# Kernel tuning notes

Measured on AMD Instinct MI355X. Metric: run time of the kernel, lower is better.

## Reference

```python
import jax, jax.numpy as jnp
import numpy as np

B, H, L, D = 2, 16, 2048, 64


def setup_inputs() -> dict:
    key = jax.random.key(0)
    kq, kk, kv = jax.random.split(key, 3)
    queries = jax.random.normal(kq, (B, H, L, D), dtype=jnp.float32)
    keys = jax.random.normal(kk, (B, H, L, D), dtype=jnp.float32)
    values = jax.random.normal(kv, (B, H, L, D), dtype=jnp.float32)
    # causal mask: True = masked (as consumed by masked_fill in the original)
    attn_mask = jnp.triu(jnp.ones((L, L), dtype=bool), k=1)
    return {"queries": queries, "keys": keys, "values": values, "attn_mask": attn_mask}


def reference(queries, keys, values, attn_mask):
    D_ = queries.shape[-1]
    scale = 1.0 / jnp.sqrt(jnp.asarray(D_, dtype=queries.dtype))
    # [B,H,Lq,Lk] score matrix (faithfully materialized as in the original)
    scores = jnp.einsum("bhqd,bhkd->bhqk", queries, keys) * scale
    scores = jnp.where(attn_mask, jnp.asarray(-1e9, dtype=scores.dtype), scores)
    attention = jax.nn.softmax(scores, axis=-1)
    # dropout rate = 0.0 (inference); identity
    out = jnp.einsum("bhqk,bhkd->bhqd", attention, values)
    return out
```

## Files before the change

### kernel.cpp

```cpp
#include <hip/hip_runtime.h>


constexpr int Lq = 2048;
constexpr int Dh = 64;
constexpr int TILEB = 16384;
constexpr int VOFF  = 8192;
constexpr size_t CNT_OFF = (size_t)32 * 32 * TILEB;
constexpr int JOBS_PER_CLASS = 256;

typedef __attribute__((ext_vector_type(16))) float f32x16;
typedef __attribute__((ext_vector_type(4))) float f32x4;
typedef __attribute__((ext_vector_type(8))) unsigned short u16x8;
typedef __attribute__((ext_vector_type(4))) unsigned int u32x4;
typedef __attribute__((ext_vector_type(8))) __bf16 bf16x8;

__device__ __forceinline__ unsigned short f2bf(float f) {
  __bf16 h = (__bf16)f;
  return __builtin_bit_cast(unsigned short, h);
}
__device__ __forceinline__ unsigned cvtpk(float lo, float hi) {
  unsigned r;
  asm("v_cvt_pk_bf16_f32 %0, %1, %2" : "=v"(r) : "v"(lo), "v"(hi));
  return r;
}
__device__ __forceinline__ f32x16 mfma32(u16x8 a, u16x8 b, f32x16 c) {
  return __builtin_amdgcn_mfma_f32_32x32x16_bf16(
      __builtin_bit_cast(bf16x8, a), __builtin_bit_cast(bf16x8, b), c, 0, 0, 0);
}
__device__ __forceinline__ void plswap(unsigned a, unsigned b,
                                       unsigned& wlo, unsigned& whi) {
#if __has_builtin(__builtin_amdgcn_permlane32_swap)
  auto r = __builtin_amdgcn_permlane32_swap((int)a, (int)b, false, false);
  wlo = (unsigned)r[0];
  whi = (unsigned)r[1];
#else
  const int hh = (threadIdx.x >> 5) & 1;
  unsigned pa = (unsigned)__shfl_xor((int)a, 32);
  unsigned pb = (unsigned)__shfl_xor((int)b, 32);
  wlo = hh ? pb : a;
  whi = hh ? b : pa;
#endif
}

__global__ __launch_bounds__(256, 2)
void repack(const float* __restrict__ K, const float* __restrict__ V,
            unsigned char* __restrict__ W, int* cnt) {
  __shared__ unsigned short Vl[64][72];

  if (cnt && blockIdx.x == 0 && threadIdx.x < 8) cnt[threadIdx.x * 64] = 0;

  const int tid = threadIdx.x;
  const int bt  = blockIdx.x;
  const int bh  = bt >> 5;
  const int tl  = bt & 31;
  const size_t src = (size_t)bh * Lq * Dh + (size_t)tl * 64 * Dh;
  unsigned char* img = W + (size_t)bt * TILEB;

  const int r  = tid >> 2;
  const int c2 = (tid & 3) * 2;

  {
    const float* kp = K + src + (size_t)r * Dh + c2 * 8;
    f32x4 a = *(const f32x4*)kp;
    f32x4 b = *(const f32x4*)(kp + 4);
    f32x4 c = *(const f32x4*)(kp + 8);
    f32x4 d = *(const f32x4*)(kp + 12);
    u16x8 lo, hi;
    #pragma unroll
    for (int jj = 0; jj < 4; ++jj) {
      lo[jj] = f2bf(a[jj]); lo[4 + jj] = f2bf(b[jj]);
      hi[jj] = f2bf(c[jj]); hi[4 + jj] = f2bf(d[jj]);
    }
    *(u16x8*)(img + (c2 * 64 + r) * 16)       = lo;
    *(u16x8*)(img + ((c2 + 1) * 64 + r) * 16) = hi;
  }
  {
    const float* vp = V + src + (size_t)r * Dh + c2 * 8;
    f32x4 a = *(const f32x4*)vp;
    f32x4 b = *(const f32x4*)(vp + 4);
    f32x4 c = *(const f32x4*)(vp + 8);
    f32x4 d = *(const f32x4*)(vp + 12);
    u16x8 lo, hi;
    #pragma unroll
    for (int jj = 0; jj < 4; ++jj) {
      lo[jj] = f2bf(a[jj]); lo[4 + jj] = f2bf(b[jj]);
      hi[jj] = f2bf(c[jj]); hi[4 + jj] = f2bf(d[jj]);
    }
    *(u16x8*)&Vl[r][c2 * 8]     = lo;
    *(u16x8*)&Vl[r][c2 * 8 + 8] = hi;
  }
  __syncthreads();
  {
    u16x8 lo, hi;
    #pragma unroll
    for (int e = 0; e < 8; ++e) {
      lo[e] = Vl[c2 * 8 + e][r];
      hi[e] = Vl[c2 * 8 + 8 + e][r];
    }
    *(u16x8*)(img + VOFF + (c2 * 64 + r) * 16)       = lo;
    *(u16x8*)(img + VOFF + ((c2 + 1) * 64 + r) * 16) = hi;
  }
}

__global__ __launch_bounds__(256, 4)
void fattn_fwd(const float* __restrict__ Q, const unsigned char* __restrict__ W,
               float* __restrict__ O, int* cnt) {
  __shared__ float Mrg[64][33];
  __shared__ int jobLDS;

  const int tid  = threadIdx.x;
  const int lane = tid & 63;
  const int w    = tid >> 6;
  const int l31  = lane & 31;
  const int h    = lane >> 5;

  const int cls  = blockIdx.x & 7;
  int* qcnt = cnt ? (cnt + cls * 64) : nullptr;

  const float QS = 0.125f * 1.4426950408889634f;
  const int laneK = ((w & 1) * 32 + l31) * 16 + h * 1024;
  const int laneV = VOFF + ((w & 1) * 4 + h) * 1024 + l31 * 16;

  for (;;) {
    int j;
    if (qcnt) {
      if (tid == 0) jobLDS = atomicAdd(qcnt, 1);
      __syncthreads();
      j = jobLDS;
    } else {
      j = blockIdx.x >> 3;
    }
    if (j >= JOBS_PER_CLASS) break;

    const int qg   = 63 - (j >> 2);
    const int bh   = cls * 4 + (j & 3);
    const int qmin = qg * 32;
    const size_t base = (size_t)bh * Lq * Dh;

    u16x8 qc[4];
    {
      const float* qp = Q + base + (size_t)(qmin + l31) * Dh + h * 8;
      #pragma unroll
      for (int dc = 0; dc < 4; ++dc) {
        f32x4 lo = *(const f32x4*)(qp + dc * 16);
        f32x4 hi = *(const f32x4*)(qp + dc * 16 + 4);
        u16x8 f;
        #pragma unroll
        for (int jj = 0; jj < 4; ++jj) {
          f[jj]     = f2bf(lo[jj] * QS);
          f[4 + jj] = f2bf(hi[jj] * QS);
        }
        qc[dc] = f;
      }
    }

    const int Sw = qg + 1 - w;
    const int nw = (Sw > 0) ? ((Sw + 3) >> 2) : 0;

    f32x16 accO0, accO1;
    #pragma unroll
    for (int i = 0; i < 16; ++i) { accO0[i] = 0.f; accO1[i] = 0.f; }
    float ls0 = 0.f, ls1 = 0.f;

    if (nw > 0) {
      const unsigned char* pT =
          W + (size_t)(bh * 32 + (w >> 1)) * TILEB;
      int kv0 = w * 32;
      for (int jj = 0; jj < nw; ++jj) {
        u16x8 kf[4], vf[4];
        {
          const unsigned char* p = pT + laneK;
          kf[0] = *(const u16x8*)(p);
          kf[1] = *(const u16x8*)(p + 2048);
          kf[2] = *(const u16x8*)(p + 4096);
          kf[3] = *(const u16x8*)(p + 6144);
        }
        {
          const unsigned char* p = pT + laneV;
          vf[0] = *(const u16x8*)(p);
          vf[1] = *(const u16x8*)(p + 512);
          vf[2] = *(const u16x8*)(p + 2048);
          vf[3] = *(const u16x8*)(p + 2560);
        }

        f32x16 s;
        #pragma unroll
        for (int i = 0; i < 16; ++i) s[i] = 0.f;
        __builtin_amdgcn_s_setprio(1);
        #pragma unroll
        for (int dc = 0; dc < 4; ++dc) s = mfma32(kf[dc], qc[dc], s);
        __builtin_amdgcn_s_setprio(0);

        float p[16];
        if (kv0 + 31 > qmin) {
          const int qrow = qmin + l31;
          #pragma unroll
          for (int r = 0; r < 16; ++r) {
            float e = __builtin_amdgcn_exp2f(s[r]);
            const int kvg = kv0 + (r & 3) + 8 * (r >> 2) + 4 * h;
            p[r] = (kvg <= qrow) ? e : 0.0f;
          }
        } else {
          #pragma unroll
          for (int r = 0; r < 16; ++r)
            p[r] = __builtin_amdgcn_exp2f(s[r]);
        }
        ls0 += ((p[0] + p[1]) + (p[2] + p[3])) + ((p[4] + p[5]) + (p[6] + p[7]));
        ls1 += ((p[8] + p[9]) + (p[10] + p[11])) + ((p[12] + p[13]) + (p[14] + p[15]));

        unsigned pk[4][2];
        #pragma unroll
        for (int q4 = 0; q4 < 4; ++q4) {
          pk[q4][0] = cvtpk(p[q4 * 4 + 0], p[q4 * 4 + 1]);
          pk[q4][1] = cvtpk(p[q4 * 4 + 2], p[q4 * 4 + 3]);
        }
        __builtin_amdgcn_s_setprio(1);
        #pragma unroll
        for (int c2 = 0; c2 < 2; ++c2) {
          unsigned w0, w1, w2, w3;
          plswap(pk[2 * c2][0], pk[2 * c2 + 1][0], w0, w2);
          plswap(pk[2 * c2][1], pk[2 * c2 + 1][1], w1, w3);
          u32x4 pw = {w0, w1, w2, w3};
          u16x8 pf = __builtin_bit_cast(u16x8, pw);
          accO0 = mfma32(vf[c2 * 2 + 0], pf, accO0);
          accO1 = mfma32(vf[c2 * 2 + 1], pf, accO1);
        }
        __builtin_amdgcn_s_setprio(0);

        pT += 2 * TILEB;
        kv0 += 128;
      }
    }

    float ls = ls0 + ls1;
    #pragma unroll
    for (int v = 1; v < 4; ++v) {
      __syncthreads();
      if (w == v) {
        float* m = &Mrg[lane][0];
        #pragma unroll
        for (int r = 0; r < 16; ++r) { m[r] = accO0[r]; m[16 + r] = accO1[r]; }
        m[32] = ls;
      }
      __syncthreads();
      if (w == 0) {
        const float* m = &Mrg[lane][0];
        #pragma unroll
        for (int r = 0; r < 16; ++r) { accO0[r] += m[r]; accO1[r] += m[16 + r]; }
        ls += m[32];
      }
    }
    if (w == 0) {
      ls += __shfl_xor(ls, 32);
      const float inv = 1.0f / ls;
      float* op = O + base + (size_t)(qmin + l31) * Dh;
      #pragma unroll
      for (int r = 0; r < 16; ++r) {
        const int d = (r & 3) + 8 * (r >> 2) + 4 * h;
        op[d]      = accO0[r] * inv;
        op[32 + d] = accO1[r] * inv;
      }
    }

    if (!qcnt) break;
  }
}

extern "C" void kernel_launch(void* const* d_in, const int* in_sizes, int n_in,
                              void* d_out, int out_size, void* d_ws, size_t ws_size,
                              hipStream_t stream) {
  const float* Q = (const float*)d_in[0];
  const float* K = (const float*)d_in[1];
  const float* V = (const float*)d_in[2];
  float* O = (float*)d_out;
  unsigned char* W = (unsigned char*)d_ws;

  int* cnt = (ws_size >= CNT_OFF + 2048) ? (int*)(W + CNT_OFF) : nullptr;

  repack<<<dim3(1024), dim3(256), 0, stream>>>(K, V, W, cnt);
  fattn_fwd<<<dim3(cnt ? 1280 : 2048), dim3(256), 0, stream>>>(Q, W, O, cnt);
}
```

Measured before the change: 49.81 us.

## Process two 32-row query groups per job to reuse K/V tile loads

Each job now covers 64 query rows as two 32-row groups sharing the same K/V fragment loads. Each loaded K/V strip feeds two QK and two PV MFMA chains, so global K/V traffic per query row is halved. The job count and grid size are halved to match, and the occupancy hint drops from 4 to 2 blocks per SIMD unit to leave room for the doubled accumulator registers. The cost is more register pressure, a larger LDS merge buffer, and fewer, larger jobs, which may hurt load balance under the causal triangle.

```diff
diff --git a/kernel.cpp b/kernel.cpp
--- a/kernel.cpp
+++ b/kernel.cpp
@@ -6,7 +6,7 @@
 constexpr int TILEB = 16384;
 constexpr int VOFF  = 8192;
 constexpr size_t CNT_OFF = (size_t)32 * 32 * TILEB;
-constexpr int JOBS_PER_CLASS = 256;
+constexpr int JOBS_PER_CLASS = 128;
 
 typedef __attribute__((ext_vector_type(16))) float f32x16;
 typedef __attribute__((ext_vector_type(4))) float f32x4;
@@ -102,10 +102,10 @@
   }
 }
 
-__global__ __launch_bounds__(256, 4)
+__global__ __launch_bounds__(256, 2)
 void fattn_fwd(const float* __restrict__ Q, const unsigned char* __restrict__ W,
                float* __restrict__ O, int* cnt) {
-  __shared__ float Mrg[64][33];
+  __shared__ float Mrg[64][66];
   __shared__ int jobLDS;
 
   const int tid  = threadIdx.x;
@@ -132,82 +132,81 @@
     }
     if (j >= JOBS_PER_CLASS) break;
 
-    const int qg   = 63 - (j >> 2);
+    const int qp   = 31 - (j >> 2);
     const int bh   = cls * 4 + (j & 3);
-    const int qmin = qg * 32;
+    const int qmA  = qp * 64;
+    const int qmB  = qmA + 32;
     const size_t base = (size_t)bh * Lq * Dh;
 
-    u16x8 qc[4];
-    {
-      const float* qp = Q + base + (size_t)(qmin + l31) * Dh + h * 8;
+    u16x8 qcA[4], qcB[4];
+    #pragma unroll
+    for (int g = 0; g < 2; ++g) {
+      const float* qp_ = Q + base + (size_t)((g ? qmB : qmA) + l31) * Dh + h * 8;
       #pragma unroll
       for (int dc = 0; dc < 4; ++dc) {
-        f32x4 lo = *(const f32x4*)(qp + dc * 16);
-        f32x4 hi = *(const f32x4*)(qp + dc * 16 + 4);
+        f32x4 lo = *(const f32x4*)(qp_ + dc * 16);
+        f32x4 hi = *(const f32x4*)(qp_ + dc * 16 + 4);
         u16x8 f;
         #pragma unroll
         for (int jj = 0; jj < 4; ++jj) {
           f[jj]     = f2bf(lo[jj] * QS);
           f[4 + jj] = f2bf(hi[jj] * QS);
         }
-        qc[dc] = f;
-      }
-    }
-
-    const int Sw = qg + 1 - w;
-    const int nw = (Sw > 0) ? ((Sw + 3) >> 2) : 0;
-
-    f32x16 accO0, accO1;
-    #pragma unroll
-    for (int i = 0; i < 16; ++i) { accO0[i] = 0.f; accO1[i] = 0.f; }
-    float ls0 = 0.f, ls1 = 0.f;
-
-    if (nw > 0) {
-      const unsigned char* pT =
-          W + (size_t)(bh * 32 + (w >> 1)) * TILEB;
-      int kv0 = w * 32;
-      for (int jj = 0; jj < nw; ++jj) {
-        u16x8 kf[4], vf[4];
-        {
-          const unsigned char* p = pT + laneK;
-          kf[0] = *(const u16x8*)(p);
-          kf[1] = *(const u16x8*)(p + 2048);
-          kf[2] = *(const u16x8*)(p + 4096);
-          kf[3] = *(const u16x8*)(p + 6144);
-        }
-        {
-          const unsigned char* p = pT + laneV;
-          vf[0] = *(const u16x8*)(p);
-          vf[1] = *(const u16x8*)(p + 512);
-          vf[2] = *(const u16x8*)(p + 2048);
-          vf[3] = *(const u16x8*)(p + 2560);
-        }
-
-        f32x16 s;
-        #pragma unroll
-        for (int i = 0; i < 16; ++i) s[i] = 0.f;
-        __builtin_amdgcn_s_setprio(1);
-        #pragma unroll
-        for (int dc = 0; dc < 4; ++dc) s = mfma32(kf[dc], qc[dc], s);
-        __builtin_amdgcn_s_setprio(0);
-
+        (g ? qcB : qcA)[dc] = f;
+      }
+    }
+
+    f32x16 aA0, aA1, aB0, aB1;
+    #pragma unroll
+    for (int i = 0; i < 16; ++i) { aA0[i] = 0.f; aA1[i] = 0.f; aB0[i] = 0.f; aB1[i] = 0.f; }
+    float lsA0 = 0.f, lsA1 = 0.f, lsB0 = 0.f, lsB1 = 0.f;
+
+    auto strip = [&](const unsigned char* pTile, int kv0,
+                     bool doA, bool maskA, bool maskB) {
+      u16x8 kf[4], vf[4];
+      {
+        const unsigned char* p = pTile + laneK;
+        kf[0] = *(const u16x8*)(p);
+        kf[1] = *(const u16x8*)(p + 2048);
+        kf[2] = *(const u16x8*)(p + 4096);
+        kf[3] = *(const u16x8*)(p + 6144);
+      }
+      {
+        const unsigned char* p = pTile + laneV;
+        vf[0] = *(const u16x8*)(p);
+        vf[1] = *(const u16x8*)(p + 512);
+        vf[2] = *(const u16x8*)(p + 2048);
+        vf[3] = *(const u16x8*)(p + 2560);
+      }
+
+      f32x16 sA, sB;
+      #pragma unroll
+      for (int i = 0; i < 16; ++i) { sA[i] = 0.f; sB[i] = 0.f; }
+      __builtin_amdgcn_s_setprio(1);
+      if (doA) {
+        #pragma unroll
+        for (int dc = 0; dc < 4; ++dc) sA = mfma32(kf[dc], qcA[dc], sA);
+      }
+      #pragma unroll
+      for (int dc = 0; dc < 4; ++dc) sB = mfma32(kf[dc], qcB[dc], sB);
+      __builtin_amdgcn_s_setprio(0);
+
+      if (doA) {
         float p[16];
-        if (kv0 + 31 > qmin) {
-          const int qrow = qmin + l31;
+        if (maskA) {
+          const int qrow = qmA + l31;
           #pragma unroll
           for (int r = 0; r < 16; ++r) {
-            float e = __builtin_amdgcn_exp2f(s[r]);
+            float e = __builtin_amdgcn_exp2f(sA[r]);
             const int kvg = kv0 + (r & 3) + 8 * (r >> 2) + 4 * h;
             p[r] = (kvg <= qrow) ? e : 0.0f;
           }
         } else {
           #pragma unroll
-          for (int r = 0; r < 16; ++r)
-            p[r] = __builtin_amdgcn_exp2f(s[r]);
-        }
-        ls0 += ((p[0] + p[1]) + (p[2] + p[3])) + ((p[4] + p[5]) + (p[6] + p[7]));
-        ls1 += ((p[8] + p[9]) + (p[10] + p[11])) + ((p[12] + p[13]) + (p[14] + p[15]));
-
+          for (int r = 0; r < 16; ++r) p[r] = __builtin_amdgcn_exp2f(sA[r]);
+        }
+        lsA0 += ((p[0] + p[1]) + (p[2] + p[3])) + ((p[4] + p[5]) + (p[6] + p[7]));
+        lsA1 += ((p[8] + p[9]) + (p[10] + p[11])) + ((p[12] + p[13]) + (p[14] + p[15]));
         unsigned pk[4][2];
         #pragma unroll
         for (int q4 = 0; q4 < 4; ++q4) {
@@ -222,43 +221,105 @@
           plswap(pk[2 * c2][1], pk[2 * c2 + 1][1], w1, w3);
           u32x4 pw = {w0, w1, w2, w3};
           u16x8 pf = __builtin_bit_cast(u16x8, pw);
-          accO0 = mfma32(vf[c2 * 2 + 0], pf, accO0);
-          accO1 = mfma32(vf[c2 * 2 + 1], pf, accO1);
+          aA0 = mfma32(vf[c2 * 2 + 0], pf, aA0);
+          aA1 = mfma32(vf[c2 * 2 + 1], pf, aA1);
         }
         __builtin_amdgcn_s_setprio(0);
-
-        pT += 2 * TILEB;
-        kv0 += 128;
-      }
-    }
-
-    float ls = ls0 + ls1;
+      }
+
+      {
+        float p[16];
+        if (maskB) {
+          const int qrow = qmB + l31;
+          #pragma unroll
+          for (int r = 0; r < 16; ++r) {
+            float e = __builtin_amdgcn_exp2f(sB[r]);
+            const int kvg = kv0 + (r & 3) + 8 * (r >> 2) + 4 * h;
+            p[r] = (kvg <= qrow) ? e : 0.0f;
+          }
+        } else {
+          #pragma unroll
+          for (int r = 0; r < 16; ++r) p[r] = __builtin_amdgcn_exp2f(sB[r]);
+        }
+        lsB0 += ((p[0] + p[1]) + (p[2] + p[3])) + ((p[4] + p[5]) + (p[6] + p[7]));
+        lsB1 += ((p[8] + p[9]) + (p[10] + p[11])) + ((p[12] + p[13]) + (p[14] + p[15]));
+        unsigned pk[4][2];
+        #pragma unroll
+        for (int q4 = 0; q4 < 4; ++q4) {
+          pk[q4][0] = cvtpk(p[q4 * 4 + 0], p[q4 * 4 + 1]);
+          pk[q4][1] = cvtpk(p[q4 * 4 + 2], p[q4 * 4 + 3]);
+        }
+        __builtin_amdgcn_s_setprio(1);
+        #pragma unroll
+        for (int c2 = 0; c2 < 2; ++c2) {
+          unsigned w0, w1, w2, w3;
+          plswap(pk[2 * c2][0], pk[2 * c2 + 1][0], w0, w2);
+          plswap(pk[2 * c2][1], pk[2 * c2 + 1][1], w1, w3);
+          u32x4 pw = {w0, w1, w2, w3};
+          u16x8 pf = __builtin_bit_cast(u16x8, pw);
+          aB0 = mfma32(vf[c2 * 2 + 0], pf, aB0);
+          aB1 = mfma32(vf[c2 * 2 + 1], pf, aB1);
+        }
+        __builtin_amdgcn_s_setprio(0);
+      }
+    };
+
+    {
+      const int num = 2 * qp - w;
+      const int nfull = (num > 0) ? ((num + 3) >> 2) : 0;
+      const unsigned char* pT = W + (size_t)(bh * 32 + (w >> 1)) * TILEB;
+      for (int t = 0; t < nfull; ++t) {
+        strip(pT, 0, true, false, false);
+        pT += 2 * (size_t)TILEB;
+      }
+    }
+    {
+      const int sD = 2 * qp;
+      if ((sD & 3) == w)
+        strip(W + (size_t)(bh * 32 + (sD >> 1)) * TILEB, 32 * sD, true, true, false);
+      const int sE = 2 * qp + 1;
+      if ((sE & 3) == w)
+        strip(W + (size_t)(bh * 32 + (sE >> 1)) * TILEB, 32 * sE, false, false, true);
+    }
+
+    float lsA = lsA0 + lsA1, lsB = lsB0 + lsB1;
     #pragma unroll
     for (int v = 1; v < 4; ++v) {
       __syncthreads();
       if (w == v) {
         float* m = &Mrg[lane][0];
         #pragma unroll
-        for (int r = 0; r < 16; ++r) { m[r] = accO0[r]; m[16 + r] = accO1[r]; }
-        m[32] = ls;
+        for (int r = 0; r < 16; ++r) {
+          m[r] = aA0[r]; m[16 + r] = aA1[r];
+          m[33 + r] = aB0[r]; m[49 + r] = aB1[r];
+        }
+        m[32] = lsA; m[65] = lsB;
       }
       __syncthreads();
       if (w == 0) {
         const float* m = &Mrg[lane][0];
         #pragma unroll
-        for (int r = 0; r < 16; ++r) { accO0[r] += m[r]; accO1[r] += m[16 + r]; }
-        ls += m[32];
+        for (int r = 0; r < 16; ++r) {
+          aA0[r] += m[r]; aA1[r] += m[16 + r];
+          aB0[r] += m[33 + r]; aB1[r] += m[49 + r];
+        }
+        lsA += m[32]; lsB += m[65];
       }
     }
     if (w == 0) {
-      ls += __shfl_xor(ls, 32);
-      const float inv = 1.0f / ls;
-      float* op = O + base + (size_t)(qmin + l31) * Dh;
+      lsA += __shfl_xor(lsA, 32);
+      lsB += __shfl_xor(lsB, 32);
+      const float invA = 1.0f / lsA;
+      const float invB = 1.0f / lsB;
+      float* opA = O + base + (size_t)(qmA + l31) * Dh;
+      float* opB = O + base + (size_t)(qmB + l31) * Dh;
       #pragma unroll
       for (int r = 0; r < 16; ++r) {
         const int d = (r & 3) + 8 * (r >> 2) + 4 * h;
-        op[d]      = accO0[r] * inv;
-        op[32 + d] = accO1[r] * inv;
+        opA[d]      = aA0[r] * invA;
+        opA[32 + d] = aA1[r] * invA;
+        opB[d]      = aB0[r] * invB;
+        opB[32 + d] = aB1[r] * invB;
       }
     }
 
@@ -278,5 +339,5 @@
   int* cnt = (ws_size >= CNT_OFF + 2048) ? (int*)(W + CNT_OFF) : nullptr;
 
   repack<<<dim3(1024), dim3(256), 0, stream>>>(K, V, W, cnt);
-  fattn_fwd<<<dim3(cnt ? 1280 : 2048), dim3(256), 0, stream>>>(Q, W, O, cnt);
-}
+  fattn_fwd<<<dim3(cnt ? 640 : 1024), dim3(256), 0, stream>>>(Q, W, O, cnt);
+}
```

Result: faster. 47.49 us (-4.7%).
